# Performance work log

Measured on AMD Instinct MI355X. Metric: run time of the kernel, lower is better.

Reference implementation:

```python
import jax, jax.numpy as jnp
import numpy as np


def setup_inputs() -> dict:
    key = jax.random.key(0)
    ks = jax.random.split(key, 5)
    B, S, D = 2, 2048, 1024
    inv = 1.0 / np.sqrt(D)
    inp = {
        "x": jax.random.normal(ks[0], (B, S, D), jnp.float32),
        "Wq": jax.random.normal(ks[1], (D, D), jnp.float32) * inv,
        "bq": jnp.zeros((D,), jnp.float32),
        "Wk": jax.random.normal(ks[2], (D, D), jnp.float32) * inv,
        "bk": jnp.zeros((D,), jnp.float32),
        "Wv": jax.random.normal(ks[3], (D, D), jnp.float32) * inv,
        "bv": jnp.zeros((D,), jnp.float32),
        "Wo": jax.random.normal(ks[4], (D, D), jnp.float32) * inv,
        "bo": jnp.zeros((D,), jnp.float32),
        "num_heads": 16,
        "window_size": 128,
    }
    return inp


def reference(x, Wq, bq, Wk, bk, Wv, bv, Wo, bo, num_heads, window_size):
    B, S, D = x.shape
    H = num_heads
    hd = D // H
    scale = 1.0 / np.sqrt(hd)

    def split_heads(t):  # [B,S,D] -> [B,H,S,hd]
        return t.reshape(B, S, H, hd).transpose(0, 2, 1, 3)

    q = split_heads(x @ Wq + bq)
    k = split_heads(x @ Wk + bk)
    v = split_heads(x @ Wv + bv)

    # dense scores, then sliding-window + causal mask (faithful to original)
    scores = jnp.einsum('bhqd,bhkd->bhqk', q, k) * scale  # [B,H,S,S]
    i = jnp.arange(S)[:, None]
    j = jnp.arange(S)[None, :]
    # position i attends to j in [i - window_size + 1, i]
    mask = (j <= i) & (j > i - window_size)
    scores = jnp.where(mask, scores, -jnp.inf)
    attn_weights = jax.nn.softmax(scores, axis=-1)  # dropout is identity in eval

    out = jnp.einsum('bhqk,bhkd->bhqd', attn_weights, v)  # [B,H,S,hd]
    out = out.transpose(0, 2, 1, 3).reshape(B, S, D)
    return out @ Wo + bo, attn_weights
```

## Files before the change

### kernel.cpp

```cpp
#include <hip/hip_runtime.h>
#include <cmath>

typedef __attribute__((ext_vector_type(8))) __bf16 v8bf;
typedef __attribute__((ext_vector_type(4))) float  v4f;

#define DEV static __device__ __forceinline__

DEV unsigned short f2bf(float f) {
  unsigned u = __builtin_bit_cast(unsigned, f);
  unsigned r = u + 0x7fffu + ((u >> 16) & 1u);
  return (unsigned short)(r >> 16);
}
DEV float bf2f(unsigned short s) {
  return __builtin_bit_cast(float, ((unsigned)s) << 16);
}
DEV v8bf ld8(const unsigned short* p) { return *(const v8bf*)p; }

__global__ __launch_bounds__(256) void k_cvt_x(const float* __restrict__ x,
                                               unsigned short* __restrict__ xb) {
  int i = blockIdx.x * 256 + threadIdx.x;
  float4 v = ((const float4*)x)[i];
  unsigned lo = (unsigned)f2bf(v.x) | ((unsigned)f2bf(v.y) << 16);
  unsigned hi = (unsigned)f2bf(v.z) | ((unsigned)f2bf(v.w) << 16);
  ((uint2*)xb)[i] = make_uint2(lo, hi);
}

__global__ __launch_bounds__(256) void k_trans_w(const float* __restrict__ src,
                                                 unsigned short* __restrict__ dst) {
  __shared__ float t[32][33];
  int n0 = blockIdx.x * 32, k0 = blockIdx.y * 32;
  int tx = threadIdx.x, ty = threadIdx.y;
  for (int r = ty; r < 32; r += 8)
    t[r][tx] = src[(k0 + r) * 1024 + n0 + tx];
  __syncthreads();
  for (int r = ty; r < 32; r += 8)
    dst[(n0 + r) * 1024 + k0 + tx] = f2bf(t[tx][r]);
}

__global__ __launch_bounds__(256) void k_bias(const float* __restrict__ bq,
                                              const float* __restrict__ bk,
                                              const float* __restrict__ bv,
                                              float* __restrict__ dst) {
  int i = blockIdx.x * 256 + threadIdx.x;
  float v = (i < 1024) ? bq[i] : (i < 2048 ? bk[i - 1024] : bv[i - 2048]);
  dst[i] = v;
}

template <bool OUT_F32>
__global__ __launch_bounds__(256) void k_gemm(const unsigned short* __restrict__ A,
                                              const unsigned short* __restrict__ Bt,
                                              const float* __restrict__ bias,
                                              void* __restrict__ Cout,
                                              int ldc) {
  constexpr int K = 1024;
  __shared__ __attribute__((aligned(16))) unsigned short As[128 * 32];
  __shared__ __attribute__((aligned(16))) unsigned short Bs[128 * 32];
  int tid = threadIdx.x;
  int wave = tid >> 6, lane = tid & 63;
  int m0 = blockIdx.y * 128, n0 = blockIdx.x * 128;
  int wm = (wave >> 1) * 64, wn = (wave & 1) * 64;
  int m = lane & 15, q4 = lane >> 4;
  int arow = tid >> 2, acol = (tid & 3) * 8;
  v4f acc[4][4] = {};
  const unsigned short* pa0 = A + (m0 + arow) * K + acol;
  const unsigned short* pa1 = A + (m0 + 64 + arow) * K + acol;
  const unsigned short* pb0 = Bt + (n0 + arow) * K + acol;
  const unsigned short* pb1 = Bt + (n0 + 64 + arow) * K + acol;

  for (int kt = 0; kt < K; kt += 32) {
    v8bf a0 = ld8(pa0 + kt), a1 = ld8(pa1 + kt);
    v8bf b0 = ld8(pb0 + kt), b1 = ld8(pb1 + kt);
    __syncthreads();
    *(v8bf*)&As[arow * 32 + acol] = a0;
    *(v8bf*)&As[(64 + arow) * 32 + acol] = a1;
    *(v8bf*)&Bs[arow * 32 + acol] = b0;
    *(v8bf*)&Bs[(64 + arow) * 32 + acol] = b1;
    __syncthreads();
    v8bf af[4], bfv[4];
#pragma unroll
    for (int mt = 0; mt < 4; mt++) af[mt] = ld8(&As[(wm + mt * 16 + m) * 32 + q4 * 8]);
#pragma unroll
    for (int nt = 0; nt < 4; nt++) bfv[nt] = ld8(&Bs[(wn + nt * 16 + m) * 32 + q4 * 8]);
#pragma unroll
    for (int mt = 0; mt < 4; mt++)
#pragma unroll
      for (int nt = 0; nt < 4; nt++)
        acc[mt][nt] = __builtin_amdgcn_mfma_f32_16x16x32_bf16(af[mt], bfv[nt], acc[mt][nt], 0, 0, 0);
  }
#pragma unroll
  for (int mt = 0; mt < 4; mt++)
#pragma unroll
    for (int nt = 0; nt < 4; nt++) {
      int col = n0 + wn + nt * 16 + m;
      float bb = bias[col];
#pragma unroll
      for (int r = 0; r < 4; r++) {
        int row = m0 + wm + mt * 16 + q4 * 4 + r;
        float v = acc[mt][nt][r] + bb;
        if (OUT_F32) ((float*)Cout)[row * ldc + col] = v;
        else ((unsigned short*)Cout)[row * ldc + col] = f2bf(v);
      }
    }
}

__global__ __launch_bounds__(256) void k_attn(const unsigned short* __restrict__ QKV,
                                              unsigned short* __restrict__ Oatt,
                                              float* __restrict__ Wout) {
  constexpr int VTS = 208;
  constexpr int PSS = 168;
  __shared__ __attribute__((aligned(16))) unsigned short Vt[64 * VTS];
  __shared__ __attribute__((aligned(16))) unsigned short Ps[4][16 * PSS];
  int b = blockIdx.z, h = blockIdx.y, i0 = blockIdx.x * 64;
  int tid = threadIdx.x, wave = tid >> 6, lane = tid & 63;
  int kbase = i0 - 128;
  const int ld = 3072;
  const unsigned short* Qg = QKV + b * 2048 * ld + h * 64;
  const unsigned short* Kg = Qg + 1024;
  const unsigned short* Vg = Qg + 2048;

  for (int c = tid; c < 192 * 16; c += 256) {
    int j = c >> 4, d0 = (c & 15) * 4;
    int jg = kbase + j; jg = jg < 0 ? 0 : jg;
    uint2 v = *(const uint2*)(Vg + jg * ld + d0);
    Vt[(d0 + 0) * VTS + j] = (unsigned short)(v.x & 0xffffu);
    Vt[(d0 + 1) * VTS + j] = (unsigned short)(v.x >> 16);
    Vt[(d0 + 2) * VTS + j] = (unsigned short)(v.y & 0xffffu);
    Vt[(d0 + 3) * VTS + j] = (unsigned short)(v.y >> 16);
  }
  for (int c = tid; c < 64 * 16; c += 256) {
    int d = c >> 4, j = 192 + (c & 15);
    Vt[d * VTS + j] = 0;
  }
  for (int c = lane; c < 16 * 24; c += 64)
    Ps[wave][(c / 24) * PSS + 144 + (c % 24)] = 0;
  __syncthreads();

  int qb = i0 + wave * 16;
  int m = lane & 15, q4 = lane >> 4;

  const unsigned short* qrow = Qg + (qb + m) * ld;
  v8bf qa0 = ld8(qrow + q4 * 8);
  v8bf qa1 = ld8(qrow + 32 + q4 * 8);

  v4f sc[9];
#pragma unroll
  for (int n = 0; n < 9; n++) {
    int key = kbase + wave * 16 + n * 16 + m;
    int kg = key < 0 ? 0 : key;
    const unsigned short* krow = Kg + kg * ld;
    v8bf kb0 = ld8(krow + q4 * 8);
    v8bf kb1 = ld8(krow + 32 + q4 * 8);
    v4f z = {0.f, 0.f, 0.f, 0.f};
    z = __builtin_amdgcn_mfma_f32_16x16x32_bf16(qa0, kb0, z, 0, 0, 0);
    z = __builtin_amdgcn_mfma_f32_16x16x32_bf16(qa1, kb1, z, 0, 0, 0);
    sc[n] = z;
  }
  float mx[4] = {-3e38f, -3e38f, -3e38f, -3e38f};
#pragma unroll
  for (int n = 0; n < 9; n++)
#pragma unroll
    for (int r = 0; r < 4; r++) {
      int i = qb + q4 * 4 + r;
      int j = kbase + wave * 16 + n * 16 + m;
      float v = sc[n][r] * 0.125f;
      bool ok = (j >= 0) && (j <= i) && (j > i - 128);
      v = ok ? v : -3e38f;
      sc[n][r] = v;
      mx[r] = fmaxf(mx[r], v);
    }
#pragma unroll
  for (int o = 1; o < 16; o <<= 1)
#pragma unroll
    for (int r = 0; r < 4; r++) mx[r] = fmaxf(mx[r], __shfl_xor(mx[r], o, 64));
  float sum[4] = {0.f, 0.f, 0.f, 0.f};
#pragma unroll
  for (int n = 0; n < 9; n++)
#pragma unroll
    for (int r = 0; r < 4; r++) {
      float p = __expf(sc[n][r] - mx[r]);
      sc[n][r] = p;
      sum[r] += p;
    }
#pragma unroll
  for (int o = 1; o < 16; o <<= 1)
#pragma unroll
    for (int r = 0; r < 4; r++) sum[r] += __shfl_xor(sum[r], o, 64);
  float inv[4];
#pragma unroll
  for (int r = 0; r < 4; r++) inv[r] = 1.0f / sum[r];

#pragma unroll
  for (int n = 0; n < 9; n++)
#pragma unroll
    for (int r = 0; r < 4; r++)
      Ps[wave][(q4 * 4 + r) * PSS + n * 16 + m] = f2bf(sc[n][r] * inv[r]);
  __syncthreads();

  v4f oacc[4] = {};
#pragma unroll
  for (int c = 0; c < 5; c++) {
    v8bf pa = ld8(&Ps[wave][m * PSS + c * 32 + q4 * 8]);
#pragma unroll
    for (int dt = 0; dt < 4; dt++) {
      v8bf vb = ld8(&Vt[(dt * 16 + m) * VTS + wave * 16 + c * 32 + q4 * 8]);
      oacc[dt] = __builtin_amdgcn_mfma_f32_16x16x32_bf16(pa, vb, oacc[dt], 0, 0, 0);
    }
  }
#pragma unroll
  for (int dt = 0; dt < 4; dt++)
#pragma unroll
    for (int r = 0; r < 4; r++)
      Oatt[(b * 2048 + qb + q4 * 4 + r) * 1024 + h * 64 + dt * 16 + m] = f2bf(oacc[dt][r]);

  float* wbase = Wout + (size_t)((b * 16 + h) * 2048) * 2048;
  for (int R = 0; R < 16; R++) {
    int i = qb + R;
    float* rowp = wbase + (size_t)i * 2048;
    int lo = i - 127;
    const unsigned short* prow = &Ps[wave][R * PSS];
    for (int it = 0; it < 8; it++) {
      int col = it * 256 + lane * 4;
      float4 v = {0.f, 0.f, 0.f, 0.f};
      if (col <= i && col + 3 >= lo) {
#pragma unroll
        for (int e = 0; e < 4; e++) {
          int j = col + e;
          if (j >= lo && j <= i && j >= 0)
            (&v.x)[e] = bf2f(prow[j - (qb - 128)]);
        }
      }
      *(float4*)(rowp + col) = v;
    }
  }
}

extern "C" void kernel_launch(void* const* d_in, const int* in_sizes, int n_in,
                              void* d_out, int out_size, void* d_ws, size_t ws_size,
                              hipStream_t stream) {
  (void)in_sizes; (void)n_in; (void)out_size; (void)ws_size;
  const float* x  = (const float*)d_in[0];
  const float* Wq = (const float*)d_in[1];
  const float* bq = (const float*)d_in[2];
  const float* Wk = (const float*)d_in[3];
  const float* bk = (const float*)d_in[4];
  const float* Wv = (const float*)d_in[5];
  const float* bv = (const float*)d_in[6];
  const float* Wo = (const float*)d_in[7];
  const float* bo = (const float*)d_in[8];

  char* ws = (char*)d_ws;
  unsigned short* xb   = (unsigned short*)(ws);
  unsigned short* WT   = (unsigned short*)(ws + 8388608);
  unsigned short* WoT  = (unsigned short*)(ws + 14680064);
  float*          bqkv = (float*)(ws + 16777216);
  unsigned short* QKV  = (unsigned short*)(ws + 16789504);
  unsigned short* Oat  = (unsigned short*)(ws + 41955328);

  float* out  = (float*)d_out;
  float* wout = out + 4194304;

  k_cvt_x<<<4096, 256, 0, stream>>>(x, xb);
  k_trans_w<<<dim3(32, 32), dim3(32, 8), 0, stream>>>(Wq, WT);
  k_trans_w<<<dim3(32, 32), dim3(32, 8), 0, stream>>>(Wk, WT + 1024 * 1024);
  k_trans_w<<<dim3(32, 32), dim3(32, 8), 0, stream>>>(Wv, WT + 2 * 1024 * 1024);
  k_trans_w<<<dim3(32, 32), dim3(32, 8), 0, stream>>>(Wo, WoT);
  k_bias<<<12, 256, 0, stream>>>(bq, bk, bv, bqkv);
  k_gemm<false><<<dim3(24, 32), 256, 0, stream>>>(xb, WT, bqkv, QKV, 3072);
  k_attn<<<dim3(32, 16, 2), 256, 0, stream>>>(QKV, Oat, wout);
  k_gemm<true><<<dim3(8, 32), 256, 0, stream>>>(Oat, WoT, bo, out, 1024);
}
```

Before: 686.2 us.

## Split attention-weight write into separate kernel, use direct-to-LDS loads in GEMM

Attention now writes only the compact 128-wide bf16 window rows of the probabilities to a workspace buffer. A new k_wwrite kernel expands these rows into the dense fp32 attention-weight matrix, which moves the large strided store out of the LDS-heavy attention kernel. The GEMM tile loads now use global_load_lds to copy straight into shared memory, and the four weight-transpose launches are merged into one. The V-transpose loop index order is also changed to alter the LDS store pattern. The costs are an extra kernel launch and an extra round trip of compact data through memory.

```diff
diff --git a/kernel.cpp b/kernel.cpp
--- a/kernel.cpp
+++ b/kernel.cpp
@@ -15,6 +15,12 @@
   return __builtin_bit_cast(float, ((unsigned)s) << 16);
 }
 DEV v8bf ld8(const unsigned short* p) { return *(const v8bf*)p; }
+
+DEV void gl16(const unsigned short* g, unsigned short* l) {
+  __builtin_amdgcn_global_load_lds(
+      (const __attribute__((address_space(1))) unsigned int*)g,
+      (__attribute__((address_space(3))) unsigned int*)l, 16, 0, 0);
+}
 
 __global__ __launch_bounds__(256) void k_cvt_x(const float* __restrict__ x,
                                                unsigned short* __restrict__ xb) {
@@ -25,11 +31,18 @@
   ((uint2*)xb)[i] = make_uint2(lo, hi);
 }
 
-__global__ __launch_bounds__(256) void k_trans_w(const float* __restrict__ src,
-                                                 unsigned short* __restrict__ dst) {
+__global__ __launch_bounds__(256) void k_trans_w4(const float* __restrict__ Wq,
+                                                  const float* __restrict__ Wk,
+                                                  const float* __restrict__ Wv,
+                                                  const float* __restrict__ Wo,
+                                                  unsigned short* __restrict__ WT,
+                                                  unsigned short* __restrict__ WoT) {
   __shared__ float t[32][33];
+  int z = blockIdx.z;
+  const float* src = (z == 0) ? Wq : (z == 1) ? Wk : (z == 2) ? Wv : Wo;
+  unsigned short* dst = (z < 3) ? WT + z * 1048576 : WoT;
   int n0 = blockIdx.x * 32, k0 = blockIdx.y * 32;
-  int tx = threadIdx.x, ty = threadIdx.y;
+  int tx = threadIdx.x & 31, ty = threadIdx.x >> 5;
   for (int r = ty; r < 32; r += 8)
     t[r][tx] = src[(k0 + r) * 1024 + n0 + tx];
   __syncthreads();
@@ -62,19 +75,20 @@
   int m = lane & 15, q4 = lane >> 4;
   int arow = tid >> 2, acol = (tid & 3) * 8;
   v4f acc[4][4] = {};
-  const unsigned short* pa0 = A + (m0 + arow) * K + acol;
-  const unsigned short* pa1 = A + (m0 + 64 + arow) * K + acol;
-  const unsigned short* pb0 = Bt + (n0 + arow) * K + acol;
-  const unsigned short* pb1 = Bt + (n0 + 64 + arow) * K + acol;
+  const unsigned short* ga0 = A + (m0 + arow) * K + acol;
+  const unsigned short* ga1 = A + (m0 + 64 + arow) * K + acol;
+  const unsigned short* gb0 = Bt + (n0 + arow) * K + acol;
+  const unsigned short* gb1 = Bt + (n0 + 64 + arow) * K + acol;
+  unsigned short* lA0 = As + wave * 512;
+  unsigned short* lA1 = As + 2048 + wave * 512;
+  unsigned short* lB0 = Bs + wave * 512;
+  unsigned short* lB1 = Bs + 2048 + wave * 512;
 
   for (int kt = 0; kt < K; kt += 32) {
-    v8bf a0 = ld8(pa0 + kt), a1 = ld8(pa1 + kt);
-    v8bf b0 = ld8(pb0 + kt), b1 = ld8(pb1 + kt);
-    __syncthreads();
-    *(v8bf*)&As[arow * 32 + acol] = a0;
-    *(v8bf*)&As[(64 + arow) * 32 + acol] = a1;
-    *(v8bf*)&Bs[arow * 32 + acol] = b0;
-    *(v8bf*)&Bs[(64 + arow) * 32 + acol] = b1;
+    gl16(ga0 + kt, lA0);
+    gl16(ga1 + kt, lA1);
+    gl16(gb0 + kt, lB0);
+    gl16(gb1 + kt, lB1);
     __syncthreads();
     v8bf af[4], bfv[4];
 #pragma unroll
@@ -86,6 +100,7 @@
 #pragma unroll
       for (int nt = 0; nt < 4; nt++)
         acc[mt][nt] = __builtin_amdgcn_mfma_f32_16x16x32_bf16(af[mt], bfv[nt], acc[mt][nt], 0, 0, 0);
+    __syncthreads();
   }
 #pragma unroll
   for (int mt = 0; mt < 4; mt++)
@@ -105,7 +120,7 @@
 
 __global__ __launch_bounds__(256) void k_attn(const unsigned short* __restrict__ QKV,
                                               unsigned short* __restrict__ Oatt,
-                                              float* __restrict__ Wout) {
+                                              unsigned short* __restrict__ cb) {
   constexpr int VTS = 208;
   constexpr int PSS = 168;
   __shared__ __attribute__((aligned(16))) unsigned short Vt[64 * VTS];
@@ -119,7 +134,9 @@
   const unsigned short* Vg = Qg + 2048;
 
   for (int c = tid; c < 192 * 16; c += 256) {
-    int j = c >> 4, d0 = (c & 15) * 4;
+    int jl = c & 15, rest = c >> 4;
+    int d0 = (rest & 15) * 4;
+    int j = (rest >> 4) * 16 + jl;
     int jg = kbase + j; jg = jg < 0 ? 0 : jg;
     uint2 v = *(const uint2*)(Vg + jg * ld + d0);
     Vt[(d0 + 0) * VTS + j] = (unsigned short)(v.x & 0xffffu);
@@ -127,10 +144,8 @@
     Vt[(d0 + 2) * VTS + j] = (unsigned short)(v.y & 0xffffu);
     Vt[(d0 + 3) * VTS + j] = (unsigned short)(v.y >> 16);
   }
-  for (int c = tid; c < 64 * 16; c += 256) {
-    int d = c >> 4, j = 192 + (c & 15);
-    Vt[d * VTS + j] = 0;
-  }
+  for (int c = tid; c < 64 * 16; c += 256)
+    Vt[(c >> 4) * VTS + 192 + (c & 15)] = 0;
   for (int c = lane; c < 16 * 24; c += 64)
     Ps[wave][(c / 24) * PSS + 144 + (c % 24)] = 0;
   __syncthreads();
@@ -212,12 +227,25 @@
     for (int r = 0; r < 4; r++)
       Oatt[(b * 2048 + qb + q4 * 4 + r) * 1024 + h * 64 + dt * 16 + m] = f2bf(oacc[dt][r]);
 
-  float* wbase = Wout + (size_t)((b * 16 + h) * 2048) * 2048;
   for (int R = 0; R < 16; R++) {
-    int i = qb + R;
-    float* rowp = wbase + (size_t)i * 2048;
+    int row = (b * 16 + h) * 2048 + qb + R;
+    unsigned short p0 = Ps[wave][R * PSS + R + 1 + lane * 2];
+    unsigned short p1 = Ps[wave][R * PSS + R + 2 + lane * 2];
+    ((unsigned*)cb)[row * 64 + lane] = (unsigned)p0 | ((unsigned)p1 << 16);
+  }
+}
+
+__global__ __launch_bounds__(256) void k_wwrite(const unsigned short* __restrict__ cb,
+                                                float* __restrict__ wout) {
+  int tid = threadIdx.x, wave = tid >> 6, lane = tid & 63;
+  int rbase = blockIdx.x * 16 + wave * 4;
+  for (int rr = 0; rr < 4; rr++) {
+    int row = rbase + rr;
+    int i = row & 2047;
+    float* rowp = wout + (size_t)row * 2048;
+    const unsigned short* crow = cb + (size_t)row * 128;
     int lo = i - 127;
-    const unsigned short* prow = &Ps[wave][R * PSS];
+#pragma unroll
     for (int it = 0; it < 8; it++) {
       int col = it * 256 + lane * 4;
       float4 v = {0.f, 0.f, 0.f, 0.f};
@@ -226,7 +254,7 @@
         for (int e = 0; e < 4; e++) {
           int j = col + e;
           if (j >= lo && j <= i && j >= 0)
-            (&v.x)[e] = bf2f(prow[j - (qb - 128)]);
+            (&v.x)[e] = bf2f(crow[j - lo]);
         }
       }
       *(float4*)(rowp + col) = v;
@@ -255,17 +283,16 @@
   float*          bqkv = (float*)(ws + 16777216);
   unsigned short* QKV  = (unsigned short*)(ws + 16789504);
   unsigned short* Oat  = (unsigned short*)(ws + 41955328);
+  unsigned short* cb   = (unsigned short*)(ws + 50343936);
 
   float* out  = (float*)d_out;
   float* wout = out + 4194304;
 
   k_cvt_x<<<4096, 256, 0, stream>>>(x, xb);
-  k_trans_w<<<dim3(32, 32), dim3(32, 8), 0, stream>>>(Wq, WT);
-  k_trans_w<<<dim3(32, 32), dim3(32, 8), 0, stream>>>(Wk, WT + 1024 * 1024);
-  k_trans_w<<<dim3(32, 32), dim3(32, 8), 0, stream>>>(Wv, WT + 2 * 1024 * 1024);
-  k_trans_w<<<dim3(32, 32), dim3(32, 8), 0, stream>>>(Wo, WoT);
+  k_trans_w4<<<dim3(32, 32, 4), 256, 0, stream>>>(Wq, Wk, Wv, Wo, WT, WoT);
   k_bias<<<12, 256, 0, stream>>>(bq, bk, bv, bqkv);
   k_gemm<false><<<dim3(24, 32), 256, 0, stream>>>(xb, WT, bqkv, QKV, 3072);
-  k_attn<<<dim3(32, 16, 2), 256, 0, stream>>>(QKV, Oat, wout);
+  k_attn<<<dim3(32, 16, 2), 256, 0, stream>>>(QKV, Oat, cb);
+  k_wwrite<<<4096, 256, 0, stream>>>(cb, wout);
   k_gemm<true><<<dim3(8, 32), 256, 0, stream>>>(Oat, WoT, bo, out, 1024);
 }
```

Result: no change. 686.5 us (+0.0%).
